# Kernel optimization log

Hardware: AMD Instinct MI355X
Metric: run time of the kernel (lower is better)

The kernel has to match this reference:

```python
import jax, jax.numpy as jnp
import numpy as np

N_NODES = 50000
N_GRAPHS = 64
HID = 128
IN_DIM = 128
N_LAYERS = 3


def setup_inputs() -> dict:
    key = jax.random.key(0)
    ks = jax.random.split(key, 12)
    x = jax.random.normal(ks[0], (N_NODES, IN_DIM), dtype=jnp.float32)
    edge_index = jax.random.randint(ks[1], (2, 800000), 0, N_NODES, dtype=jnp.int64)
    batch = jnp.sort(jax.random.randint(ks[2], (N_NODES,), 0, N_GRAPHS, dtype=jnp.int64))
    s = 1.0 / np.sqrt(HID)
    W0 = jax.random.normal(ks[3], (IN_DIM, HID), dtype=jnp.float32) * s
    b0 = jnp.zeros((HID,), dtype=jnp.float32)
    Ws = jax.random.normal(ks[4], (N_LAYERS, HID, HID), dtype=jnp.float32) * s
    bs = jnp.zeros((N_LAYERS, HID), dtype=jnp.float32)
    W1 = jax.random.normal(ks[5], (HID, HID // 2), dtype=jnp.float32) * s
    b1 = jnp.zeros((HID // 2,), dtype=jnp.float32)
    W2 = jax.random.normal(ks[6], (HID // 2, 2), dtype=jnp.float32) * (1.0 / np.sqrt(HID // 2))
    b2 = jnp.zeros((2,), dtype=jnp.float32)
    return {"x": x, "edge_index": edge_index, "batch": batch,
            "W0": W0, "b0": b0, "Ws": Ws, "bs": bs,
            "W1": W1, "b1": b1, "W2": W2, "b2": b2}


def reference(x, edge_index, batch, W0, b0, Ws, bs, W1, b1, W2, b2):
    n = x.shape[0]
    # GCN: add self-loops, symmetric normalization D^-1/2 (A+I) D^-1/2
    loop = jnp.arange(n, dtype=edge_index.dtype)
    src = jnp.concatenate([edge_index[0], loop])  # [E+N]
    dst = jnp.concatenate([edge_index[1], loop])
    deg = jax.ops.segment_sum(jnp.ones_like(dst, dtype=x.dtype), dst, num_segments=n)
    dinv = jax.lax.rsqrt(jnp.maximum(deg, 1.0))
    coef = (dinv[src] * dinv[dst])[:, None]  # [E+N, 1]

    def gcn(h, W, b):
        hw = h @ W                                  # transform first (cheaper)
        agg = jax.ops.segment_sum(hw[src] * coef, dst, num_segments=n)
        return jax.nn.relu(agg + b)

    h = gcn(x, W0, b0)
    for i in range(Ws.shape[0]):
        h = gcn(h, Ws[i], bs[i])

    # global mean pool over graphs
    sums = jax.ops.segment_sum(h, batch, num_segments=N_GRAPHS)
    cnts = jax.ops.segment_sum(jnp.ones((n,), dtype=h.dtype), batch, num_segments=N_GRAPHS)
    pooled = sums / jnp.maximum(cnts, 1.0)[:, None]  # [G, HID]

    out = jax.nn.relu(pooled @ W1 + b1) @ W2 + b2    # [G, 2]
    return out
```

## Files before the change

### kernel.cpp

```cpp
#include <hip/hip_runtime.h>
#include <hip/hip_bf16.h>
#include <hip/hip_fp16.h>

#define HID 128
#define N_GRAPHS 64

typedef _Float16 h8 __attribute__((ext_vector_type(8)));
typedef float f4 __attribute__((ext_vector_type(4)));

__global__ void init_deg_kernel(int* __restrict__ deg, int n) {
    int i = blockIdx.x * 256 + threadIdx.x;
    if (i < n) deg[i] = 1;
}

__global__ void count_kernel(const int* __restrict__ dst, int* __restrict__ deg, int E) {
    int e = blockIdx.x * 256 + threadIdx.x;
    if (e < E) atomicAdd(&deg[dst[e]], 1);
}

__global__ __launch_bounds__(256) void scan_partial_kernel(const int* __restrict__ deg,
                                                           int* __restrict__ bsum, int n) {
    __shared__ int red[256];
    int t = threadIdx.x;
    int i = blockIdx.x * 256 + t;
    red[t] = (i < n) ? deg[i] : 0;
    __syncthreads();
#pragma unroll
    for (int s = 128; s > 0; s >>= 1) {
        if (t < s) red[t] += red[t + s];
        __syncthreads();
    }
    if (t == 0) bsum[blockIdx.x] = red[0];
}

__global__ __launch_bounds__(256) void scan_bsum_kernel(const int* __restrict__ bsum,
                                                        int* __restrict__ boff,
                                                        int* __restrict__ row_ptr,
                                                        int nb, int n) {
    __shared__ int arr[256];
    int t = threadIdx.x;
    int own = (t < nb) ? bsum[t] : 0;
    arr[t] = own;
    __syncthreads();
#pragma unroll
    for (int off = 1; off < 256; off <<= 1) {
        int v = arr[t];
        int add = (t >= off) ? arr[t - off] : 0;
        __syncthreads();
        arr[t] = v + add;
        __syncthreads();
    }
    if (t < nb) boff[t] = arr[t] - own;
    if (t == 255) row_ptr[n] = arr[255];
}

__global__ __launch_bounds__(256) void scan_emit_kernel(const int* __restrict__ deg,
                                                        const int* __restrict__ boff,
                                                        int* __restrict__ row_ptr,
                                                        int* __restrict__ cursor,
                                                        float* __restrict__ dinv, int n) {
    __shared__ int arr[256];
    int t = threadIdx.x;
    int i = blockIdx.x * 256 + t;
    int d = (i < n) ? deg[i] : 0;
    arr[t] = d;
    __syncthreads();
#pragma unroll
    for (int off = 1; off < 256; off <<= 1) {
        int v = arr[t];
        int add = (t >= off) ? arr[t - off] : 0;
        __syncthreads();
        arr[t] = v + add;
        __syncthreads();
    }
    if (i < n) {
        int pos = boff[blockIdx.x] + arr[t] - d;
        row_ptr[i] = pos;
        cursor[i] = pos;
        dinv[i] = rsqrtf((float)d);
    }
}

__global__ __launch_bounds__(256) void fill_kernel(const int* __restrict__ src,
                                                   const int* __restrict__ dst,
                                                   int* __restrict__ cursor,
                                                   int* __restrict__ col,
                                                   int E, int n) {
    int r = blockIdx.x & 7;
    int sub = blockIdx.x >> 3;
    int nsub = gridDim.x >> 3;
    int rw = (n + 7) / 8;
    int lo = r * rw;
    int hi = lo + rw; if (hi > n) hi = n;
    int t = threadIdx.x;
    for (int e = sub * 256 + t; e < E; e += nsub * 256) {
        int d = dst[e];
        if (d >= lo && d < hi) {
            int pos = atomicAdd(&cursor[d], 1);
            col[pos] = src[e];
        }
    }
    for (int v = lo + sub * 256 + t; v < hi; v += nsub * 256) {
        int pos = atomicAdd(&cursor[v], 1);
        col[pos] = v;
    }
}

__global__ void cvt_kernel(const float* __restrict__ in, __half* __restrict__ out, int total8) {
    int i = blockIdx.x * 256 + threadIdx.x;
    if (i >= total8) return;
    float4 v0 = *(const float4*)(in + (size_t)i * 8);
    float4 v1 = *(const float4*)(in + (size_t)i * 8 + 4);
    __half2 p0 = __floats2half2_rn(v0.x, v0.y);
    __half2 p1 = __floats2half2_rn(v0.z, v0.w);
    __half2 p2 = __floats2half2_rn(v1.x, v1.y);
    __half2 p3 = __floats2half2_rn(v1.z, v1.w);
    float4 pk;
    ((__half2*)&pk)[0] = p0; ((__half2*)&pk)[1] = p1;
    ((__half2*)&pk)[2] = p2; ((__half2*)&pk)[3] = p3;
    *(float4*)(out + (size_t)i * 8) = pk;
}

__global__ __launch_bounds__(256) void gemm_mfma_kernel(const __half* __restrict__ A16,
                                                        const float* __restrict__ W,
                                                        const float* __restrict__ dinv,
                                                        __half* __restrict__ out16, int M) {
    __shared__ _Float16 sWt[128][136];
    int tid = threadIdx.x;
    for (int i = tid * 4; i < 128 * 128; i += 1024) {
        int k = i >> 7, nn = i & 127;
        float4 v = *(const float4*)(W + i);
        sWt[nn + 0][k] = (_Float16)v.x;
        sWt[nn + 1][k] = (_Float16)v.y;
        sWt[nn + 2][k] = (_Float16)v.z;
        sWt[nn + 3][k] = (_Float16)v.w;
    }
    __syncthreads();

    int wave = tid >> 6;
    int lane = tid & 63;
    int l15 = lane & 15;
    int kg = lane >> 4;
    int rowb = blockIdx.x * 64 + wave * 16;
    int arow = rowb + l15;

    h8 zero;
#pragma unroll
    for (int q = 0; q < 8; ++q) zero[q] = (_Float16)0.f;

    h8 afrag[4];
    if (arow < M) {
        const h8* Av = (const h8*)(A16 + (size_t)arow * 128 + kg * 8);
#pragma unroll
        for (int kc = 0; kc < 4; ++kc) afrag[kc] = Av[kc * 4];
    } else {
#pragma unroll
        for (int kc = 0; kc < 4; ++kc) afrag[kc] = zero;
    }

    int orow0 = rowb + kg * 4;
    float dv[4];
#pragma unroll
    for (int j = 0; j < 4; ++j)
        dv[j] = (orow0 + j < M) ? dinv[orow0 + j] : 0.f;

    for (int ct = 0; ct < 8; ++ct) {
        h8 bfrag[4];
#pragma unroll
        for (int kc = 0; kc < 4; ++kc)
            bfrag[kc] = *(const h8*)&sWt[ct * 16 + l15][kc * 32 + kg * 8];
        f4 acc = {0.f, 0.f, 0.f, 0.f};
#pragma unroll
        for (int kc = 0; kc < 4; ++kc)
            acc = __builtin_amdgcn_mfma_f32_16x16x32_f16(afrag[kc], bfrag[kc], acc, 0, 0, 0);
#pragma unroll
        for (int j = 0; j < 4; ++j) {
            int r = orow0 + j;
            if (r < M)
                out16[(size_t)r * 128 + ct * 16 + l15] = __float2half(acc[j] * dv[j]);
        }
    }
}

__global__ __launch_bounds__(256) void aggregate_kernel(const __half* __restrict__ hw,
                                                        const int* __restrict__ row_ptr,
                                                        const int* __restrict__ col,
                                                        const float* __restrict__ dinv,
                                                        const float* __restrict__ bias,
                                                        __half* __restrict__ out16, int n) {
    int tid = threadIdx.x;
    int v = blockIdx.x * 16 + (tid >> 4);
    if (v >= n) return;
    int j = (tid & 15) * 8;
    int p0 = row_ptr[v], p1 = row_ptr[v + 1];
    float acc[8];
#pragma unroll
    for (int q = 0; q < 8; ++q) acc[q] = 0.f;

    int p = p0;
    for (; p + 3 < p1; p += 4) {
        int s0 = col[p], s1 = col[p + 1], s2 = col[p + 2], s3 = col[p + 3];
        float4 r0 = *(const float4*)(hw + (size_t)s0 * 128 + j);
        float4 r1 = *(const float4*)(hw + (size_t)s1 * 128 + j);
        float4 r2 = *(const float4*)(hw + (size_t)s2 * 128 + j);
        float4 r3 = *(const float4*)(hw + (size_t)s3 * 128 + j);
        const __half2* h0 = (const __half2*)&r0;
        const __half2* h1 = (const __half2*)&r1;
        const __half2* h2 = (const __half2*)&r2;
        const __half2* h3 = (const __half2*)&r3;
#pragma unroll
        for (int q = 0; q < 4; ++q) {
            float2 f0 = __half22float2(h0[q]);
            float2 f1 = __half22float2(h1[q]);
            float2 f2 = __half22float2(h2[q]);
            float2 f3 = __half22float2(h3[q]);
            acc[2 * q + 0] += (f0.x + f1.x) + (f2.x + f3.x);
            acc[2 * q + 1] += (f0.y + f1.y) + (f2.y + f3.y);
        }
    }
    for (; p < p1; ++p) {
        int s0 = col[p];
        float4 r0 = *(const float4*)(hw + (size_t)s0 * 128 + j);
        const __half2* h0 = (const __half2*)&r0;
#pragma unroll
        for (int q = 0; q < 4; ++q) {
            float2 f0 = __half22float2(h0[q]);
            acc[2 * q + 0] += f0.x;
            acc[2 * q + 1] += f0.y;
        }
    }
    float dv = dinv[v];
    float4 bb0 = *(const float4*)(bias + j);
    float4 bb1 = *(const float4*)(bias + j + 4);
    float r[8];
    r[0] = fmaxf(acc[0] * dv + bb0.x, 0.f);
    r[1] = fmaxf(acc[1] * dv + bb0.y, 0.f);
    r[2] = fmaxf(acc[2] * dv + bb0.z, 0.f);
    r[3] = fmaxf(acc[3] * dv + bb0.w, 0.f);
    r[4] = fmaxf(acc[4] * dv + bb1.x, 0.f);
    r[5] = fmaxf(acc[5] * dv + bb1.y, 0.f);
    r[6] = fmaxf(acc[6] * dv + bb1.z, 0.f);
    r[7] = fmaxf(acc[7] * dv + bb1.w, 0.f);
    float4 pk;
    ((__half2*)&pk)[0] = __floats2half2_rn(r[0], r[1]);
    ((__half2*)&pk)[1] = __floats2half2_rn(r[2], r[3]);
    ((__half2*)&pk)[2] = __floats2half2_rn(r[4], r[5]);
    ((__half2*)&pk)[3] = __floats2half2_rn(r[6], r[7]);
    *(float4*)(out16 + (size_t)v * 128 + j) = pk;
}

__global__ void boundary_kernel(const int* __restrict__ batch, int* __restrict__ start, int n) {
    int i = blockIdx.x * 256 + threadIdx.x;
    if (i >= n) return;
    int b = batch[i];
    int pb = (i > 0) ? batch[i - 1] : -1;
    if (b != pb) {
        for (int g = pb + 1; g <= b; ++g) start[g] = i;
    }
    if (i == n - 1) {
        for (int g = b + 1; g <= N_GRAPHS; ++g) start[g] = n;
    }
}

__global__ __launch_bounds__(256) void pool_reduce_kernel(const __half* __restrict__ h,
                                                          const int* __restrict__ start,
                                                          float* __restrict__ pooled) {
    __shared__ float part[8][128];
    int g = blockIdx.x;
    int s = start[g], e = start[g + 1];
    int tid = threadIdx.x;
    int grp = tid >> 5;
    int j = (tid & 31) * 4;
    float4 acc = make_float4(0.f, 0.f, 0.f, 0.f);
    for (int v = s + grp; v < e; v += 8) {
        float2 raw = *(const float2*)(h + (size_t)v * 128 + j);
        float2 f0 = __half22float2(((const __half2*)&raw)[0]);
        float2 f1 = __half22float2(((const __half2*)&raw)[1]);
        acc.x += f0.x; acc.y += f0.y; acc.z += f1.x; acc.w += f1.y;
    }
    *(float4*)&part[grp][j] = acc;
    __syncthreads();
    if (tid < 128) {
        float sum = 0.f;
#pragma unroll
        for (int k = 0; k < 8; ++k) sum += part[k][tid];
        int cntv = e - s; if (cntv < 1) cntv = 1;
        pooled[g * 128 + tid] = sum / (float)cntv;
    }
}

__global__ __launch_bounds__(256) void mlp_kernel(const float* __restrict__ pooled_g,
                                                  const float* __restrict__ W1,
                                                  const float* __restrict__ b1,
                                                  const float* __restrict__ W2,
                                                  const float* __restrict__ b2,
                                                  float* __restrict__ out) {
    __shared__ float pooled[64][128];
    __shared__ float h1[64][64];
    int tid = threadIdx.x;
    for (int i = tid; i < 64 * 128; i += 256) pooled[i >> 7][i & 127] = pooled_g[i];
    __syncthreads();
    for (int i = tid; i < 64 * 64; i += 256) {
        int g = i >> 6, j = i & 63;
        float acc = b1[j];
        for (int k = 0; k < 128; ++k) acc += pooled[g][k] * W1[k * 64 + j];
        h1[g][j] = fmaxf(acc, 0.f);
    }
    __syncthreads();
    if (tid < 128) {
        int g = tid >> 1, c = tid & 1;
        float acc = b2[c];
        for (int jj = 0; jj < 64; ++jj) acc += h1[g][jj] * W2[jj * 2 + c];
        out[tid] = acc;
    }
}

extern "C" void kernel_launch(void* const* d_in, const int* in_sizes, int n_in,
                              void* d_out, int out_size, void* d_ws, size_t ws_size,
                              hipStream_t stream) {
    const float* x    = (const float*)d_in[0];
    const int*   ei   = (const int*)d_in[1];
    const int*   batch= (const int*)d_in[2];
    const float* W0   = (const float*)d_in[3];
    const float* b0   = (const float*)d_in[4];
    const float* Ws   = (const float*)d_in[5];
    const float* bs   = (const float*)d_in[6];
    const float* W1   = (const float*)d_in[7];
    const float* b1   = (const float*)d_in[8];
    const float* W2   = (const float*)d_in[9];
    const float* b2   = (const float*)d_in[10];
    float* out = (float*)d_out;

    const int n  = in_sizes[0] / HID;
    const int E  = in_sizes[1] / 2;
    const int EN = E + n;
    const int* src = ei;
    const int* dst = ei + E;
    const int nb = (n + 255) / 256;

    char* ws = (char*)d_ws;
    size_t off = 0;
    auto alloc = [&](size_t bytes) { void* p = ws + off; off = (off + bytes + 255) & ~(size_t)255; return p; };
    __half* h16    = (__half*)alloc((size_t)n * HID * 2);
    __half* hw16   = (__half*)alloc((size_t)n * HID * 2);
    float*  dinv   = (float*) alloc((size_t)n * 4);
    int*    row_ptr= (int*)   alloc((size_t)(n + 1) * 4);
    int*    cursor = (int*)   alloc((size_t)n * 4);
    int*    deg    = (int*)   alloc((size_t)n * 4);
    int*    col    = (int*)   alloc((size_t)EN * 4);
    int*    bsum   = (int*)   alloc((size_t)nb * 4);
    int*    boff   = (int*)   alloc((size_t)nb * 4);
    int*    gstart = (int*)   alloc((N_GRAPHS + 1) * 4);
    float*  pooled = (float*) alloc(N_GRAPHS * 128 * 4);
    (void)ws_size; (void)n_in; (void)out_size;

    init_deg_kernel<<<nb, 256, 0, stream>>>(deg, n);
    count_kernel<<<(E + 255) / 256, 256, 0, stream>>>(dst, deg, E);
    scan_partial_kernel<<<nb, 256, 0, stream>>>(deg, bsum, n);
    scan_bsum_kernel<<<1, 256, 0, stream>>>(bsum, boff, row_ptr, nb, n);
    scan_emit_kernel<<<nb, 256, 0, stream>>>(deg, boff, row_ptr, cursor, dinv, n);
    fill_kernel<<<512, 256, 0, stream>>>(src, dst, cursor, col, E, n);
    boundary_kernel<<<nb, 256, 0, stream>>>(batch, gstart, n);
    cvt_kernel<<<(n * HID / 8 + 255) / 256, 256, 0, stream>>>(x, h16, n * HID / 8);

    const int gemm_grid = (n + 63) / 64;
    const int node_grid = (n + 15) / 16;

    gemm_mfma_kernel<<<gemm_grid, 256, 0, stream>>>(h16, W0, dinv, hw16, n);
    aggregate_kernel<<<node_grid, 256, 0, stream>>>(hw16, row_ptr, col, dinv, b0, h16, n);
    for (int l = 0; l < 3; ++l) {
        gemm_mfma_kernel<<<gemm_grid, 256, 0, stream>>>(h16, Ws + (size_t)l * HID * HID, dinv, hw16, n);
        aggregate_kernel<<<node_grid, 256, 0, stream>>>(hw16, row_ptr, col, dinv, bs + (size_t)l * HID, h16, n);
    }

    pool_reduce_kernel<<<N_GRAPHS, 256, 0, stream>>>(h16, gstart, pooled);
    mlp_kernel<<<1, 256, 0, stream>>>(pooled, W1, b1, W2, b2, out);
}
```

Baseline: 446.5 us.

## Partition degree counting by node range, double GEMM rows per wave, enlarge fill grid

The degree-count kernel now has eight groups of blocks each own one slice of destination node IDs and scan every edge. Atomics for a slice therefore land in a narrower address range, at the cost of reading the edge list eight times. The self-loop +1 moves from initialisation into the scan kernels. The GEMM kernel processes 32 rows per wave (two 16-row MFMA tiles sharing the B fragments), which halves the grid and the per-block LDS weight loads. The fill kernel grid also grows from 512 to 2048 blocks.

New measurement: 416.8 us. 6.7% less time.

```diff
diff --git a/kernel.cpp b/kernel.cpp
--- a/kernel.cpp
+++ b/kernel.cpp
@@ -10,12 +10,21 @@
 
 __global__ void init_deg_kernel(int* __restrict__ deg, int n) {
     int i = blockIdx.x * 256 + threadIdx.x;
-    if (i < n) deg[i] = 1;
-}
-
-__global__ void count_kernel(const int* __restrict__ dst, int* __restrict__ deg, int E) {
-    int e = blockIdx.x * 256 + threadIdx.x;
-    if (e < E) atomicAdd(&deg[dst[e]], 1);
+    if (i < n) deg[i] = 0;
+}
+
+__global__ __launch_bounds__(256) void count_kernel(const int* __restrict__ dst,
+                                                    int* __restrict__ deg, int E, int n) {
+    int r = blockIdx.x & 7;
+    int sub = blockIdx.x >> 3;
+    int nsub = gridDim.x >> 3;
+    int rw = (n + 7) / 8;
+    int lo = r * rw;
+    int hi = lo + rw; if (hi > n) hi = n;
+    for (int e = sub * 256 + threadIdx.x; e < E; e += nsub * 256) {
+        int d = dst[e];
+        if (d >= lo && d < hi) atomicAdd(&deg[d], 1);
+    }
 }
 
 __global__ __launch_bounds__(256) void scan_partial_kernel(const int* __restrict__ deg,
@@ -23,7 +32,7 @@
     __shared__ int red[256];
     int t = threadIdx.x;
     int i = blockIdx.x * 256 + t;
-    red[t] = (i < n) ? deg[i] : 0;
+    red[t] = (i < n) ? deg[i] + 1 : 0;
     __syncthreads();
 #pragma unroll
     for (int s = 128; s > 0; s >>= 1) {
@@ -62,7 +71,7 @@
     __shared__ int arr[256];
     int t = threadIdx.x;
     int i = blockIdx.x * 256 + t;
-    int d = (i < n) ? deg[i] : 0;
+    int d = (i < n) ? deg[i] + 1 : 0;
     arr[t] = d;
     __syncthreads();
 #pragma unroll
@@ -141,43 +150,61 @@
     int lane = tid & 63;
     int l15 = lane & 15;
     int kg = lane >> 4;
-    int rowb = blockIdx.x * 64 + wave * 16;
-    int arow = rowb + l15;
+    int rowb = blockIdx.x * 128 + wave * 32;
+    int arowA = rowb + l15;
+    int arowB = rowb + 16 + l15;
 
     h8 zero;
 #pragma unroll
     for (int q = 0; q < 8; ++q) zero[q] = (_Float16)0.f;
 
-    h8 afrag[4];
-    if (arow < M) {
-        const h8* Av = (const h8*)(A16 + (size_t)arow * 128 + kg * 8);
-#pragma unroll
-        for (int kc = 0; kc < 4; ++kc) afrag[kc] = Av[kc * 4];
+    h8 afragA[4], afragB[4];
+    if (arowA < M) {
+        const h8* Av = (const h8*)(A16 + (size_t)arowA * 128 + kg * 8);
+#pragma unroll
+        for (int kc = 0; kc < 4; ++kc) afragA[kc] = Av[kc * 4];
     } else {
 #pragma unroll
-        for (int kc = 0; kc < 4; ++kc) afrag[kc] = zero;
-    }
-
-    int orow0 = rowb + kg * 4;
-    float dv[4];
-#pragma unroll
-    for (int j = 0; j < 4; ++j)
-        dv[j] = (orow0 + j < M) ? dinv[orow0 + j] : 0.f;
+        for (int kc = 0; kc < 4; ++kc) afragA[kc] = zero;
+    }
+    if (arowB < M) {
+        const h8* Av = (const h8*)(A16 + (size_t)arowB * 128 + kg * 8);
+#pragma unroll
+        for (int kc = 0; kc < 4; ++kc) afragB[kc] = Av[kc * 4];
+    } else {
+#pragma unroll
+        for (int kc = 0; kc < 4; ++kc) afragB[kc] = zero;
+    }
+
+    int orowA = rowb + kg * 4;
+    int orowB = rowb + 16 + kg * 4;
+    float dvA[4], dvB[4];
+#pragma unroll
+    for (int j = 0; j < 4; ++j) {
+        dvA[j] = (orowA + j < M) ? dinv[orowA + j] : 0.f;
+        dvB[j] = (orowB + j < M) ? dinv[orowB + j] : 0.f;
+    }
 
     for (int ct = 0; ct < 8; ++ct) {
         h8 bfrag[4];
 #pragma unroll
         for (int kc = 0; kc < 4; ++kc)
             bfrag[kc] = *(const h8*)&sWt[ct * 16 + l15][kc * 32 + kg * 8];
-        f4 acc = {0.f, 0.f, 0.f, 0.f};
-#pragma unroll
-        for (int kc = 0; kc < 4; ++kc)
-            acc = __builtin_amdgcn_mfma_f32_16x16x32_f16(afrag[kc], bfrag[kc], acc, 0, 0, 0);
+        f4 accA = {0.f, 0.f, 0.f, 0.f};
+        f4 accB = {0.f, 0.f, 0.f, 0.f};
+#pragma unroll
+        for (int kc = 0; kc < 4; ++kc) {
+            accA = __builtin_amdgcn_mfma_f32_16x16x32_f16(afragA[kc], bfrag[kc], accA, 0, 0, 0);
+            accB = __builtin_amdgcn_mfma_f32_16x16x32_f16(afragB[kc], bfrag[kc], accB, 0, 0, 0);
+        }
 #pragma unroll
         for (int j = 0; j < 4; ++j) {
-            int r = orow0 + j;
-            if (r < M)
-                out16[(size_t)r * 128 + ct * 16 + l15] = __float2half(acc[j] * dv[j]);
+            int rA = orowA + j;
+            if (rA < M)
+                out16[(size_t)rA * 128 + ct * 16 + l15] = __float2half(accA[j] * dvA[j]);
+            int rB = orowB + j;
+            if (rB < M)
+                out16[(size_t)rB * 128 + ct * 16 + l15] = __float2half(accB[j] * dvB[j]);
         }
     }
 }
@@ -333,10 +360,10 @@
 
     const int n  = in_sizes[0] / HID;
     const int E  = in_sizes[1] / 2;
-    const int EN = E + n;
     const int* src = ei;
     const int* dst = ei + E;
     const int nb = (n + 255) / 256;
+    const int EN = E + n;
 
     char* ws = (char*)d_ws;
     size_t off = 0;
@@ -355,15 +382,15 @@
     (void)ws_size; (void)n_in; (void)out_size;
 
     init_deg_kernel<<<nb, 256, 0, stream>>>(deg, n);
-    count_kernel<<<(E + 255) / 256, 256, 0, stream>>>(dst, deg, E);
+    count_kernel<<<2048, 256, 0, stream>>>(dst, deg, E, n);
     scan_partial_kernel<<<nb, 256, 0, stream>>>(deg, bsum, n);
     scan_bsum_kernel<<<1, 256, 0, stream>>>(bsum, boff, row_ptr, nb, n);
     scan_emit_kernel<<<nb, 256, 0, stream>>>(deg, boff, row_ptr, cursor, dinv, n);
-    fill_kernel<<<512, 256, 0, stream>>>(src, dst, cursor, col, E, n);
+    fill_kernel<<<2048, 256, 0, stream>>>(src, dst, cursor, col, E, n);
     boundary_kernel<<<nb, 256, 0, stream>>>(batch, gstart, n);
     cvt_kernel<<<(n * HID / 8 + 255) / 256, 256, 0, stream>>>(x, h16, n * HID / 8);
 
-    const int gemm_grid = (n + 63) / 64;
+    const int gemm_grid = (n + 127) / 128;
     const int node_grid = (n + 15) / 16;
 
     gemm_mfma_kernel<<<gemm_grid, 256, 0, stream>>>(h16, W0, dinv, hw16, n);
```
